# Kernel tuning notes

Measured on AMD Instinct MI355X. Metric: run time of the kernel, lower is better.

## Reference

```python
import jax, jax.numpy as jnp
import numpy as np
from jax.scipy.special import logsumexp

HEAD = 12
EPS = 1.0


def _sinkhorn(dots):
    # dots: [b, h, n, n]. Faithful to the torch code: eps=1, max_iter=3,
    # update order u, v, u (the err<1e-6 early-break never triggers for
    # unconverged random-scale inputs, so we unroll the 3 iterations).
    C = -dots
    b, h, n, m = C.shape
    log_mu = -jnp.log(jnp.asarray(n, dtype=C.dtype))  # log(1/n)
    log_nu = -jnp.log(jnp.asarray(m, dtype=C.dtype))
    u = jnp.zeros((b, h, n), dtype=C.dtype)
    v = jnp.zeros((b, h, m), dtype=C.dtype)

    def M(u, v):
        # (-C + u_i + v_j) / eps
        return (-C + u[..., :, None] + v[..., None, :]) / EPS

    # i = 0: row update
    u = EPS * (log_mu - logsumexp(M(u, v), axis=-1)) + u
    # i = 1: column update (logsumexp over transpose == axis=-2)
    v = EPS * (log_nu - logsumexp(M(u, v), axis=-2)) + v
    # i = 2: row update
    u = EPS * (log_mu - logsumexp(M(u, v), axis=-1)) + u
    return jnp.exp(M(u, v))


def setup_inputs() -> dict:
    key = jax.random.key(0)
    ks = jax.random.split(key, 6)
    b, n, f = 8, 1024, 768
    x = jax.random.normal(ks[0], (b, n, f), dtype=jnp.float32)
    s = 1.0 / np.sqrt(f)
    Wq = jax.random.normal(ks[1], (f, f), dtype=jnp.float32) * s
    Wk = jax.random.normal(ks[2], (f, f), dtype=jnp.float32) * s
    Wv = jax.random.normal(ks[3], (f, f), dtype=jnp.float32) * s
    Wo = jax.random.normal(ks[4], (f, f), dtype=jnp.float32) * s
    bo = jax.random.normal(ks[5], (f,), dtype=jnp.float32) * 0.01
    return {"x": x, "Wq": Wq, "Wk": Wk, "Wv": Wv, "Wo": Wo, "bo": bo}


def reference(x, Wq, Wk, Wv, Wo, bo):
    b, n, f = x.shape
    h = HEAD
    d = f // h
    scale = d ** (-0.5)
    # nn.Linear: y = x @ W.T
    q = (x @ Wq.T).reshape(b, n, h, d).transpose(0, 2, 1, 3)  # [b,h,n,d]
    k = (x @ Wk.T).reshape(b, n, h, d).transpose(0, 2, 1, 3)
    v = (x @ Wv.T).reshape(b, n, h, d).transpose(0, 2, 1, 3)
    dots = jnp.einsum("bhid,bhjd->bhij", q, k) * scale  # [b,h,n,n]
    attn = _sinkhorn(dots)
    out = jnp.einsum("bhij,bhjd->bhid", attn, v)
    out = out.transpose(0, 2, 1, 3).reshape(b, n, f)
    return out @ Wo.T + bo
```

## Files before the change

kernel.cpp:

```cpp
#include <hip/hip_runtime.h>

#define DEV __device__ __forceinline__

typedef __attribute__((ext_vector_type(4))) float f32x4;
typedef __attribute__((ext_vector_type(16))) float f32x16;
typedef __attribute__((ext_vector_type(8))) short bf16x8;
typedef __attribute__((ext_vector_type(4))) short bf16x4;

DEV short f2bf(float f) {
    union { float f; unsigned u; } v; v.f = f;
    unsigned r = (v.u + 0x7fffu + ((v.u >> 16) & 1u)) >> 16;
    return (short)r;
}

#ifndef __has_builtin
#define __has_builtin(x) 0
#endif
#if __has_builtin(__builtin_amdgcn_cvt_pk_bf16_f32)
DEV unsigned pkbf(float a, float b) {
    auto r = __builtin_amdgcn_cvt_pk_bf16_f32(a, b);
    union { __typeof__(r) v; unsigned u; } u; u.v = r; return u.u;
}
#else
DEV unsigned pkbf(float a, float b) {
    return (unsigned)(unsigned short)f2bf(a) | ((unsigned)(unsigned short)f2bf(b) << 16);
}
#endif

DEV void gl_lds16(const void* g, void* l) {
    __builtin_amdgcn_global_load_lds(
        (__attribute__((address_space(1))) void*)(g),
        (__attribute__((address_space(3))) void*)(l), 16, 0, 0);
}

template <int ITERS>
DEV void stage_tile(const short* g, int ldg, short* lds, int t) {
    const int w = t >> 6;
#pragma unroll
    for (int it = 0; it < ITERS; ++it) {
        int row = it * 32 + (t >> 3);
        int cx = (t & 7) ^ ((t >> 3) & 7);
        gl_lds16(g + row * ldg + cx * 8, (char*)lds + it * 4096 + (w << 10));
    }
}

DEV bf16x8 ldfrag(const short* lds, int r, int kc) {
    return *(const bf16x8*)(lds + r * 64 + ((kc ^ (r & 7)) << 3));
}

DEV bf16x4 ldv4(const short* lds, int r, int o) {
    int chunk = o >> 3, sub = o & 7;
    return *(const bf16x4*)(lds + r * 64 + ((chunk ^ (r & 7)) << 3) + sub);
}

__global__ void cvt_all(const float* __restrict__ x,
                        const float* __restrict__ wq, const float* __restrict__ wk,
                        const float* __restrict__ wv, const float* __restrict__ wo,
                        short* __restrict__ xb,
                        short* __restrict__ wqb, short* __restrict__ wkb,
                        short* __restrict__ wvb, short* __restrict__ wob) {
    int b = blockIdx.x;
    const float* s; short* d; int i;
    if (b < 6144) {
        s = x; d = xb; i = b * 256 + threadIdx.x;
    } else {
        int r = b - 6144;
        int wi = r / 576, rem = r - wi * 576;
        s = (wi == 0) ? wq : (wi == 1) ? wk : (wi == 2) ? wv : wo;
        d = (wi == 0) ? wqb : (wi == 1) ? wkb : (wi == 2) ? wvb : wob;
        i = rem * 256 + threadIdx.x;
    }
    float4 v = ((const float4*)s)[i];
    short4 o;
    o.x = f2bf(v.x); o.y = f2bf(v.y); o.z = f2bf(v.z); o.w = f2bf(v.w);
    ((short4*)d)[i] = o;
}

#define TSTRIDE 136
__global__ __launch_bounds__(256, 4) void proj_gemm(
    const short* __restrict__ xb,
    const short* __restrict__ wq, const short* __restrict__ wk, const short* __restrict__ wv,
    short* __restrict__ Qg, short* __restrict__ Kg, short* __restrict__ Vtg)
{
    __shared__ __align__(16) char smem[128 * TSTRIDE * 2];
    short* At = (short*)smem;
    short* Bt = (short*)(smem + 128 * 64 * 2);
    short* Ct = (short*)smem;
    const int t = threadIdx.x;
    const int z = blockIdx.z;
    const int row0 = blockIdx.x * 128, col0 = blockIdx.y * 128;
    const int lane = t & 63, w = t >> 6;
    const int l31 = lane & 31, lh = lane >> 5;
    const int wm = w >> 1, wn = w & 1;
    const short* W = (z == 0) ? wq : (z == 1) ? wk : wv;

    f32x16 acc[2][2];
#pragma unroll
    for (int i = 0; i < 2; ++i)
#pragma unroll
        for (int j = 0; j < 2; ++j) acc[i][j] = (f32x16)(0.f);

    for (int k0 = 0; k0 < 768; k0 += 64) {
        __syncthreads();
        stage_tile<4>(xb + (size_t)row0 * 768 + k0, 768, At, t);
        stage_tile<4>(W + (size_t)col0 * 768 + k0, 768, Bt, t);
        __syncthreads();
#pragma unroll
        for (int s = 0; s < 4; ++s) {
            bf16x8 af[2], bfr[2];
#pragma unroll
            for (int tm = 0; tm < 2; ++tm) af[tm] = ldfrag(At, wm * 64 + tm * 32 + l31, s * 2 + lh);
#pragma unroll
            for (int tn = 0; tn < 2; ++tn) bfr[tn] = ldfrag(Bt, wn * 64 + tn * 32 + l31, s * 2 + lh);
#pragma unroll
            for (int tm = 0; tm < 2; ++tm)
#pragma unroll
                for (int tn = 0; tn < 2; ++tn)
                    acc[tm][tn] = __builtin_amdgcn_mfma_f32_32x32x16_bf16(af[tm], bfr[tn], acc[tm][tn], 0, 0, 0);
        }
    }

    __syncthreads();
    if (z == 2) {
#pragma unroll
        for (int tm = 0; tm < 2; ++tm)
#pragma unroll
            for (int tn = 0; tn < 2; ++tn) {
                int ddl = wn * 64 + tn * 32 + l31;
#pragma unroll
                for (int g = 0; g < 4; ++g) {
                    int rrl = wm * 64 + tm * 32 + 8 * g + 4 * lh;
                    short4 v4;
                    v4.x = f2bf(acc[tm][tn][4 * g + 0]);
                    v4.y = f2bf(acc[tm][tn][4 * g + 1]);
                    v4.z = f2bf(acc[tm][tn][4 * g + 2]);
                    v4.w = f2bf(acc[tm][tn][4 * g + 3]);
                    *(short4*)(Ct + ddl * TSTRIDE + rrl) = v4;
                }
            }
    } else {
        const float sc = (z == 0) ? 0.125f * 1.4426950408889634f : 1.0f;
#pragma unroll
        for (int tm = 0; tm < 2; ++tm)
#pragma unroll
            for (int tn = 0; tn < 2; ++tn) {
                int ddl = wn * 64 + tn * 32 + l31;
#pragma unroll
                for (int reg = 0; reg < 16; ++reg) {
                    int rrl = wm * 64 + tm * 32 + (reg & 3) + 8 * (reg >> 2) + 4 * lh;
                    Ct[rrl * TSTRIDE + ddl] = f2bf(acc[tm][tn][reg] * sc);
                }
            }
    }
    __syncthreads();

    const int bb = row0 >> 10;
#pragma unroll
    for (int it = 0; it < 8; ++it) {
        int row = it * 16 + (t >> 4);
        int ck = t & 15;
        bf16x8 v = *(const bf16x8*)(Ct + row * TSTRIDE + ck * 8);
        if (z == 2) {
            int gdd = col0 + row;
            int head = bb * 12 + (gdd >> 6);
            *(bf16x8*)(Vtg + ((size_t)head * 64 + (gdd & 63)) * 1024 + (row0 & 1023) + ck * 8) = v;
        } else {
            int rr = (row0 & 1023) + row;
            int gc = col0 + ck * 8;
            int head = bb * 12 + (gc >> 6);
            short* dst = (z == 0) ? Qg : Kg;
            *(bf16x8*)(dst + ((size_t)head * 1024 + rr) * 64 + (gc & 63)) = v;
        }
    }
}

__global__ __launch_bounds__(256) void lse_pass(
    const short* __restrict__ Aall, const short* __restrict__ Ball,
    const float* __restrict__ bias, float* __restrict__ outv,
    float bias_sign, float out_sign)
{
    __shared__ __align__(16) short At[128 * 64];
    __shared__ __align__(16) short Bt[128 * 64];
    __shared__ __align__(16) float biasl[1024];
    const int t = threadIdx.x;
    const int head = blockIdx.x % 96;
    const int r0 = (blockIdx.x / 96) * 128;
    const int lane = t & 63, w = t >> 6, quad = lane >> 4, c = lane & 15;
    const short* A = Aall + (size_t)head * 65536;
    const short* B = Ball + (size_t)head * 65536;

    stage_tile<4>(A + r0 * 64, 64, At, t);
    if (bias) {
        float4 v = ((const float4*)(bias + (size_t)head * 1024))[t];
        v.x *= bias_sign; v.y *= bias_sign; v.z *= bias_sign; v.w *= bias_sign;
        ((float4*)biasl)[t] = v;
    } else ((float4*)biasl)[t] = make_float4(0.f, 0.f, 0.f, 0.f);

    float lsum[2] = {0.f, 0.f};

    for (int j0 = 0; j0 < 1024; j0 += 128) {
        __syncthreads();
        stage_tile<4>(B + j0 * 64, 64, Bt, t);
        __syncthreads();
        f32x4 sacc[8][2];
#pragma unroll
        for (int fm = 0; fm < 8; ++fm)
#pragma unroll
            for (int fn = 0; fn < 2; ++fn) sacc[fm][fn] = (f32x4){0.f, 0.f, 0.f, 0.f};
#pragma unroll
        for (int ks = 0; ks < 2; ++ks) {
            bf16x8 af[8], bfr[2];
#pragma unroll
            for (int fm = 0; fm < 8; ++fm) af[fm] = ldfrag(Bt, fm * 16 + c, ks * 4 + quad);
#pragma unroll
            for (int fn = 0; fn < 2; ++fn) bfr[fn] = ldfrag(At, w * 32 + fn * 16 + c, ks * 4 + quad);
#pragma unroll
            for (int fm = 0; fm < 8; ++fm)
#pragma unroll
                for (int fn = 0; fn < 2; ++fn)
                    sacc[fm][fn] = __builtin_amdgcn_mfma_f32_16x16x32_bf16(af[fm], bfr[fn], sacc[fm][fn], 0, 0, 0);
        }
#pragma unroll
        for (int fm = 0; fm < 8; ++fm) {
            float4 b4 = *(const float4*)(biasl + j0 + fm * 16 + quad * 4);
#pragma unroll
            for (int fn = 0; fn < 2; ++fn) {
                float p0 = __builtin_amdgcn_exp2f(sacc[fm][fn][0] + b4.x);
                float p1 = __builtin_amdgcn_exp2f(sacc[fm][fn][1] + b4.y);
                float p2 = __builtin_amdgcn_exp2f(sacc[fm][fn][2] + b4.z);
                float p3 = __builtin_amdgcn_exp2f(sacc[fm][fn][3] + b4.w);
                lsum[fn] += (p0 + p1) + (p2 + p3);
            }
        }
    }

#pragma unroll
    for (int fn = 0; fn < 2; ++fn) {
        float s = lsum[fn];
        s += __shfl_xor(s, 16); s += __shfl_xor(s, 32);
        lsum[fn] = s;
    }
    if (quad == 0 && w < 4) {
#pragma unroll
        for (int fn = 0; fn < 2; ++fn)
            outv[(size_t)head * 1024 + r0 + w * 32 + fn * 16 + c] =
                out_sign * __builtin_amdgcn_logf(lsum[fn]);
    }
}

__global__ __launch_bounds__(256, 4) void flash_pass(
    const short* __restrict__ Qall, const short* __restrict__ Kall,
    const short* __restrict__ Vtall, const float* __restrict__ v1,
    short* __restrict__ ctx)
{
    __shared__ __align__(16) short Qt[128 * 64];
    __shared__ __align__(16) short Kt[64 * 64];
    __shared__ __align__(16) short Vtl[64 * 64];
    __shared__ __align__(16) float v1l[1024];
    const int t = threadIdx.x;
    const int head = blockIdx.x % 96;
    const int r0 = (blockIdx.x / 96) * 128;
    const int lane = t & 63, w = t >> 6, quad = lane >> 4, c = lane & 15;
    const short* Q = Qall + (size_t)head * 65536;
    const short* K = Kall + (size_t)head * 65536;
    const short* Vt = Vtall + (size_t)head * 65536;

    stage_tile<4>(Q + r0 * 64, 64, Qt, t);
    ((float4*)v1l)[t] = ((const float4*)(v1 + (size_t)head * 1024))[t];

    float lsum[2] = {0.f, 0.f};
    f32x4 oacc[4][2];
#pragma unroll
    for (int md = 0; md < 4; ++md)
#pragma unroll
        for (int ni = 0; ni < 2; ++ni) oacc[md][ni] = (f32x4){0.f, 0.f, 0.f, 0.f};

    for (int j0 = 0; j0 < 1024; j0 += 64) {
        __syncthreads();
        stage_tile<2>(K + j0 * 64, 64, Kt, t);
        stage_tile<2>(Vt + j0, 1024, Vtl, t);
        __syncthreads();
        f32x4 sacc[4][2];
#pragma unroll
        for (int fm = 0; fm < 4; ++fm)
#pragma unroll
            for (int fn = 0; fn < 2; ++fn) sacc[fm][fn] = (f32x4){0.f, 0.f, 0.f, 0.f};
#pragma unroll
        for (int ks = 0; ks < 2; ++ks) {
            bf16x8 af[4], bfr[2];
#pragma unroll
            for (int fm = 0; fm < 4; ++fm) af[fm] = ldfrag(Kt, fm * 16 + c, ks * 4 + quad);
#pragma unroll
            for (int fn = 0; fn < 2; ++fn) bfr[fn] = ldfrag(Qt, w * 32 + fn * 16 + c, ks * 4 + quad);
#pragma unroll
            for (int fm = 0; fm < 4; ++fm)
#pragma unroll
                for (int fn = 0; fn < 2; ++fn)
                    sacc[fm][fn] = __builtin_amdgcn_mfma_f32_16x16x32_bf16(af[fm], bfr[fn], sacc[fm][fn], 0, 0, 0);
        }
        unsigned pk[4][2][2];
#pragma unroll
        for (int fm = 0; fm < 4; ++fm) {
            float4 b4 = *(const float4*)(v1l + j0 + fm * 16 + quad * 4);
#pragma unroll
            for (int fn = 0; fn < 2; ++fn) {
                float p0 = __builtin_amdgcn_exp2f(sacc[fm][fn][0] + b4.x);
                float p1 = __builtin_amdgcn_exp2f(sacc[fm][fn][1] + b4.y);
                float p2 = __builtin_amdgcn_exp2f(sacc[fm][fn][2] + b4.z);
                float p3 = __builtin_amdgcn_exp2f(sacc[fm][fn][3] + b4.w);
                lsum[fn] += (p0 + p1) + (p2 + p3);
                pk[fm][fn][0] = pkbf(p0, p1);
                pk[fm][fn][1] = pkbf(p2, p3);
            }
        }
#pragma unroll
        for (int ks = 0; ks < 2; ++ks) {
            bf16x8 vaf[4];
#pragma unroll
            for (int md = 0; md < 4; ++md) {
                union { bf16x8 v8; bf16x4 h[2]; } u;
                u.h[0] = ldv4(Vtl, md * 16 + c, ks * 32 + quad * 4);
                u.h[1] = ldv4(Vtl, md * 16 + c, ks * 32 + 16 + quad * 4);
                vaf[md] = u.v8;
            }
#pragma unroll
            for (int ni = 0; ni < 2; ++ni) {
                union { bf16x8 v8; unsigned u4[4]; } b;
                b.u4[0] = pk[2 * ks + 0][ni][0];
                b.u4[1] = pk[2 * ks + 0][ni][1];
                b.u4[2] = pk[2 * ks + 1][ni][0];
                b.u4[3] = pk[2 * ks + 1][ni][1];
#pragma unroll
                for (int md = 0; md < 4; ++md)
                    oacc[md][ni] = __builtin_amdgcn_mfma_f32_16x16x32_bf16(vaf[md], b.v8, oacc[md][ni], 0, 0, 0);
            }
        }
    }

#pragma unroll
    for (int fn = 0; fn < 2; ++fn) {
        float s = lsum[fn];
        s += __shfl_xor(s, 16); s += __shfl_xor(s, 32);
        lsum[fn] = s;
    }
    const int bb = head / 12, hh = head % 12;
#pragma unroll
    for (int ni = 0; ni < 2; ++ni) {
        float nrm = __builtin_amdgcn_rcpf(1024.f * lsum[ni]);
        int rr = r0 + w * 32 + ni * 16 + c;
#pragma unroll
        for (int md = 0; md < 4; ++md) {
            short4 v4;
            v4.x = f2bf(oacc[md][ni][0] * nrm);
            v4.y = f2bf(oacc[md][ni][1] * nrm);
            v4.z = f2bf(oacc[md][ni][2] * nrm);
            v4.w = f2bf(oacc[md][ni][3] * nrm);
            *(short4*)(ctx + ((size_t)(bb * 1024 + rr)) * 768 + hh * 64 + md * 16 + quad * 4) = v4;
        }
    }
}

__global__ __launch_bounds__(256, 4) void out_gemm(
    const short* __restrict__ ctxb, const short* __restrict__ wo,
    const float* __restrict__ bo, float* __restrict__ out)
{
    __shared__ __align__(16) short At[128 * 64];
    __shared__ __align__(16) short Bt[128 * 64];
    const int t = threadIdx.x;
    const int row0 = blockIdx.x * 128, col0 = blockIdx.y * 128;
    const int lane = t & 63, w = t >> 6;
    const int l31 = lane & 31, lh = lane >> 5;
    const int wm = w >> 1, wn = w & 1;

    f32x16 acc[2][2];
#pragma unroll
    for (int i = 0; i < 2; ++i)
#pragma unroll
        for (int j = 0; j < 2; ++j) acc[i][j] = (f32x16)(0.f);

    for (int k0 = 0; k0 < 768; k0 += 64) {
        __syncthreads();
        stage_tile<4>(ctxb + (size_t)row0 * 768 + k0, 768, At, t);
        stage_tile<4>(wo + (size_t)col0 * 768 + k0, 768, Bt, t);
        __syncthreads();
#pragma unroll
        for (int s = 0; s < 4; ++s) {
            bf16x8 af[2], bfr[2];
#pragma unroll
            for (int tm = 0; tm < 2; ++tm) af[tm] = ldfrag(At, wm * 64 + tm * 32 + l31, s * 2 + lh);
#pragma unroll
            for (int tn = 0; tn < 2; ++tn) bfr[tn] = ldfrag(Bt, wn * 64 + tn * 32 + l31, s * 2 + lh);
#pragma unroll
            for (int tm = 0; tm < 2; ++tm)
#pragma unroll
                for (int tn = 0; tn < 2; ++tn)
                    acc[tm][tn] = __builtin_amdgcn_mfma_f32_32x32x16_bf16(af[tm], bfr[tn], acc[tm][tn], 0, 0, 0);
        }
    }
#pragma unroll
    for (int tm = 0; tm < 2; ++tm)
#pragma unroll
        for (int tn = 0; tn < 2; ++tn) {
            int gc = col0 + wn * 64 + tn * 32 + l31;
            float b = bo[gc];
#pragma unroll
            for (int reg = 0; reg < 16; ++reg) {
                int gr = row0 + wm * 64 + tm * 32 + (reg & 3) + 8 * (reg >> 2) + 4 * lh;
                out[(size_t)gr * 768 + gc] = acc[tm][tn][reg] + b;
            }
        }
}

extern "C" void kernel_launch(void* const* d_in, const int* in_sizes, int n_in,
                              void* d_out, int out_size, void* d_ws, size_t ws_size,
                              hipStream_t stream) {
    const float* x  = (const float*)d_in[0];
    const float* Wq = (const float*)d_in[1];
    const float* Wk = (const float*)d_in[2];
    const float* Wv = (const float*)d_in[3];
    const float* Wo = (const float*)d_in[4];
    const float* bo = (const float*)d_in[5];
    float* out = (float*)d_out;

    char* p = (char*)d_ws;
    short* xb  = (short*)p; p += (size_t)8192 * 768 * 2;
    short* wqb = (short*)p; p += (size_t)768 * 768 * 2;
    short* wkb = (short*)p; p += (size_t)768 * 768 * 2;
    short* wvb = (short*)p; p += (size_t)768 * 768 * 2;
    short* wob = (short*)p; p += (size_t)768 * 768 * 2;
    short* Qg  = (short*)p; p += (size_t)96 * 1024 * 64 * 2;
    short* Kg  = (short*)p; p += (size_t)96 * 1024 * 64 * 2;
    short* Vtg = (short*)p; p += (size_t)96 * 1024 * 64 * 2;
    float* r1  = (float*)p; p += (size_t)96 * 1024 * 4;
    float* v1  = (float*)p; p += (size_t)96 * 1024 * 4;
    short* ctx = (short*)p; p += (size_t)8192 * 768 * 2;

    cvt_all<<<6144 + 4 * 576, 256, 0, stream>>>(x, Wq, Wk, Wv, Wo, xb, wqb, wkb, wvb, wob);

    proj_gemm<<<dim3(64, 6, 3), 256, 0, stream>>>(xb, wqb, wkb, wvb, Qg, Kg, Vtg);

    lse_pass<<<768, 256, 0, stream>>>(Qg, Kg, nullptr, r1, 0.f, 1.f);
    lse_pass<<<768, 256, 0, stream>>>(Kg, Qg, r1, v1, -1.f, -1.f);

    flash_pass<<<768, 256, 0, stream>>>(Qg, Kg, Vtg, v1, ctx);

    out_gemm<<<dim3(64, 6), 256, 0, stream>>>(ctx, wob, bo, out);
}
```

Baseline: 242.1 us.

## Permute V layout for single-fragment loads, fold bias into MFMA init, halve LSE tiles

```diff
diff --git a/kernel.cpp b/kernel.cpp
--- a/kernel.cpp
+++ b/kernel.cpp
@@ -46,11 +46,6 @@
 
 DEV bf16x8 ldfrag(const short* lds, int r, int kc) {
     return *(const bf16x8*)(lds + r * 64 + ((kc ^ (r & 7)) << 3));
-}
-
-DEV bf16x4 ldv4(const short* lds, int r, int o) {
-    int chunk = o >> 3, sub = o & 7;
-    return *(const bf16x4*)(lds + r * 64 + ((chunk ^ (r & 7)) << 3) + sub);
 }
 
 __global__ void cvt_all(const float* __restrict__ x,
@@ -130,12 +125,14 @@
 #pragma unroll
                 for (int g = 0; g < 4; ++g) {
                     int rrl = wm * 64 + tm * 32 + 8 * g + 4 * lh;
+                    int j6 = rrl & 63;
+                    int pp = (rrl & ~63) | (j6 & 32) | ((j6 & 12) << 1) | ((j6 & 16) >> 2);
                     short4 v4;
                     v4.x = f2bf(acc[tm][tn][4 * g + 0]);
                     v4.y = f2bf(acc[tm][tn][4 * g + 1]);
                     v4.z = f2bf(acc[tm][tn][4 * g + 2]);
                     v4.w = f2bf(acc[tm][tn][4 * g + 3]);
-                    *(short4*)(Ct + ddl * TSTRIDE + rrl) = v4;
+                    *(short4*)(Ct + ddl * TSTRIDE + pp) = v4;
                 }
             }
     } else {
@@ -174,78 +171,65 @@
     }
 }
 
-__global__ __launch_bounds__(256) void lse_pass(
+__global__ __launch_bounds__(256, 5) void lse_pass(
     const short* __restrict__ Aall, const short* __restrict__ Ball,
     const float* __restrict__ bias, float* __restrict__ outv,
     float bias_sign, float out_sign)
 {
-    __shared__ __align__(16) short At[128 * 64];
+    __shared__ __align__(16) short At[64 * 64];
     __shared__ __align__(16) short Bt[128 * 64];
     __shared__ __align__(16) float biasl[1024];
     const int t = threadIdx.x;
     const int head = blockIdx.x % 96;
-    const int r0 = (blockIdx.x / 96) * 128;
+    const int r0 = (blockIdx.x / 96) * 64;
     const int lane = t & 63, w = t >> 6, quad = lane >> 4, c = lane & 15;
     const short* A = Aall + (size_t)head * 65536;
     const short* B = Ball + (size_t)head * 65536;
 
-    stage_tile<4>(A + r0 * 64, 64, At, t);
+    stage_tile<2>(A + r0 * 64, 64, At, t);
     if (bias) {
         float4 v = ((const float4*)(bias + (size_t)head * 1024))[t];
         v.x *= bias_sign; v.y *= bias_sign; v.z *= bias_sign; v.w *= bias_sign;
         ((float4*)biasl)[t] = v;
     } else ((float4*)biasl)[t] = make_float4(0.f, 0.f, 0.f, 0.f);
 
-    float lsum[2] = {0.f, 0.f};
+    float lsum = 0.f;
 
     for (int j0 = 0; j0 < 1024; j0 += 128) {
         __syncthreads();
         stage_tile<4>(B + j0 * 64, 64, Bt, t);
         __syncthreads();
-        f32x4 sacc[8][2];
-#pragma unroll
-        for (int fm = 0; fm < 8; ++fm)
-#pragma unroll
-            for (int fn = 0; fn < 2; ++fn) sacc[fm][fn] = (f32x4){0.f, 0.f, 0.f, 0.f};
-#pragma unroll
-        for (int ks = 0; ks < 2; ++ks) {
-            bf16x8 af[8], bfr[2];
-#pragma unroll
-            for (int fm = 0; fm < 8; ++fm) af[fm] = ldfrag(Bt, fm * 16 + c, ks * 4 + quad);
-#pragma unroll
-            for (int fn = 0; fn < 2; ++fn) bfr[fn] = ldfrag(At, w * 32 + fn * 16 + c, ks * 4 + quad);
-#pragma unroll
-            for (int fm = 0; fm < 8; ++fm)
-#pragma unroll
-                for (int fn = 0; fn < 2; ++fn)
-                    sacc[fm][fn] = __builtin_amdgcn_mfma_f32_16x16x32_bf16(af[fm], bfr[fn], sacc[fm][fn], 0, 0, 0);
-        }
+        f32x4 sacc[8];
 #pragma unroll
         for (int fm = 0; fm < 8; ++fm) {
             float4 b4 = *(const float4*)(biasl + j0 + fm * 16 + quad * 4);
-#pragma unroll
-            for (int fn = 0; fn < 2; ++fn) {
-                float p0 = __builtin_amdgcn_exp2f(sacc[fm][fn][0] + b4.x);
-                float p1 = __builtin_amdgcn_exp2f(sacc[fm][fn][1] + b4.y);
-                float p2 = __builtin_amdgcn_exp2f(sacc[fm][fn][2] + b4.z);
-                float p3 = __builtin_amdgcn_exp2f(sacc[fm][fn][3] + b4.w);
-                lsum[fn] += (p0 + p1) + (p2 + p3);
-            }
-        }
-    }
-
-#pragma unroll
-    for (int fn = 0; fn < 2; ++fn) {
-        float s = lsum[fn];
-        s += __shfl_xor(s, 16); s += __shfl_xor(s, 32);
-        lsum[fn] = s;
-    }
-    if (quad == 0 && w < 4) {
-#pragma unroll
-        for (int fn = 0; fn < 2; ++fn)
-            outv[(size_t)head * 1024 + r0 + w * 32 + fn * 16 + c] =
-                out_sign * __builtin_amdgcn_logf(lsum[fn]);
-    }
+            sacc[fm] = (f32x4){b4.x, b4.y, b4.z, b4.w};
+        }
+#pragma unroll
+        for (int ks = 0; ks < 2; ++ks) {
+            bf16x8 af[8], bfr;
+#pragma unroll
+            for (int fm = 0; fm < 8; ++fm) af[fm] = ldfrag(Bt, fm * 16 + c, ks * 4 + quad);
+            bfr = ldfrag(At, w * 16 + c, ks * 4 + quad);
+#pragma unroll
+            for (int fm = 0; fm < 8; ++fm)
+                sacc[fm] = __builtin_amdgcn_mfma_f32_16x16x32_bf16(af[fm], bfr, sacc[fm], 0, 0, 0);
+        }
+#pragma unroll
+        for (int fm = 0; fm < 8; ++fm) {
+            float p0 = __builtin_amdgcn_exp2f(sacc[fm][0]);
+            float p1 = __builtin_amdgcn_exp2f(sacc[fm][1]);
+            float p2 = __builtin_amdgcn_exp2f(sacc[fm][2]);
+            float p3 = __builtin_amdgcn_exp2f(sacc[fm][3]);
+            lsum += (p0 + p1) + (p2 + p3);
+        }
+    }
+
+    lsum += __shfl_xor(lsum, 16);
+    lsum += __shfl_xor(lsum, 32);
+    if (quad == 0)
+        outv[(size_t)head * 1024 + r0 + w * 16 + c] =
+            out_sign * __builtin_amdgcn_logf(lsum);
 }
 
 __global__ __launch_bounds__(256, 4) void flash_pass(
@@ -282,9 +266,11 @@
         __syncthreads();
         f32x4 sacc[4][2];
 #pragma unroll
-        for (int fm = 0; fm < 4; ++fm)
-#pragma unroll
-            for (int fn = 0; fn < 2; ++fn) sacc[fm][fn] = (f32x4){0.f, 0.f, 0.f, 0.f};
+        for (int fm = 0; fm < 4; ++fm) {
+            float4 b4 = *(const float4*)(v1l + j0 + fm * 16 + quad * 4);
+#pragma unroll
+            for (int fn = 0; fn < 2; ++fn) sacc[fm][fn] = (f32x4){b4.x, b4.y, b4.z, b4.w};
+        }
 #pragma unroll
         for (int ks = 0; ks < 2; ++ks) {
             bf16x8 af[4], bfr[2];
@@ -300,29 +286,22 @@
         }
         unsigned pk[4][2][2];
 #pragma unroll
-        for (int fm = 0; fm < 4; ++fm) {
-            float4 b4 = *(const float4*)(v1l + j0 + fm * 16 + quad * 4);
+        for (int fm = 0; fm < 4; ++fm)
 #pragma unroll
             for (int fn = 0; fn < 2; ++fn) {
-                float p0 = __builtin_amdgcn_exp2f(sacc[fm][fn][0] + b4.x);
-                float p1 = __builtin_amdgcn_exp2f(sacc[fm][fn][1] + b4.y);
-                float p2 = __builtin_amdgcn_exp2f(sacc[fm][fn][2] + b4.z);
-                float p3 = __builtin_amdgcn_exp2f(sacc[fm][fn][3] + b4.w);
+                float p0 = __builtin_amdgcn_exp2f(sacc[fm][fn][0]);
+                float p1 = __builtin_amdgcn_exp2f(sacc[fm][fn][1]);
+                float p2 = __builtin_amdgcn_exp2f(sacc[fm][fn][2]);
+                float p3 = __builtin_amdgcn_exp2f(sacc[fm][fn][3]);
                 lsum[fn] += (p0 + p1) + (p2 + p3);
                 pk[fm][fn][0] = pkbf(p0, p1);
                 pk[fm][fn][1] = pkbf(p2, p3);
             }
-        }
 #pragma unroll
         for (int ks = 0; ks < 2; ++ks) {
             bf16x8 vaf[4];
 #pragma unroll
-            for (int md = 0; md < 4; ++md) {
-                union { bf16x8 v8; bf16x4 h[2]; } u;
-                u.h[0] = ldv4(Vtl, md * 16 + c, ks * 32 + quad * 4);
-                u.h[1] = ldv4(Vtl, md * 16 + c, ks * 32 + 16 + quad * 4);
-                vaf[md] = u.v8;
-            }
+            for (int md = 0; md < 4; ++md) vaf[md] = ldfrag(Vtl, md * 16 + c, ks * 4 + quad);
 #pragma unroll
             for (int ni = 0; ni < 2; ++ni) {
                 union { bf16x8 v8; unsigned u4[4]; } b;
@@ -439,8 +418,8 @@
 
     proj_gemm<<<dim3(64, 6, 3), 256, 0, stream>>>(xb, wqb, wkb, wvb, Qg, Kg, Vtg);
 
-    lse_pass<<<768, 256, 0, stream>>>(Qg, Kg, nullptr, r1, 0.f, 1.f);
-    lse_pass<<<768, 256, 0, stream>>>(Kg, Qg, r1, v1, -1.f, -1.f);
+    lse_pass<<<1536, 256, 0, stream>>>(Qg, Kg, nullptr, r1, 0.f, 1.f);
+    lse_pass<<<1536, 256, 0, stream>>>(Kg, Qg, r1, v1, -1.f, -1.f);
 
     flash_pass<<<768, 256, 0, stream>>>(Qg, Kg, Vtg, v1, ctx);
 
```

After: 218.5 us. 9.8% less time.
